# Kernel tuning notes

Measured on AMD Instinct MI355X. Metric: run time of the kernel, lower is better.

Reference implementation:

```python
import jax, jax.numpy as jnp
import numpy as np

N = 50000   # nodes
E = 800000  # edges
H = 128     # hidden_channels
L = 3       # num_layers - 2 GIN blocks
C = 1       # out_channels
G = 512     # graphs in batch
BN_EPS = 1e-5


def _bn(x, g, b, m, v):
    # BatchNorm1d in eval mode: running stats
    return g * (x - m) * jax.lax.rsqrt(v + BN_EPS) + b


def setup_inputs() -> dict:
    key = jax.random.key(0)
    ks = jax.random.split(key, 16)
    s = 0.05
    inp = {
        "x": jax.random.randint(ks[0], (N,), 0, 100),
        "edge_index": jax.random.randint(ks[1], (2, E), 0, N),
        "batch": jnp.sort(jax.random.randint(ks[2], (N,), 0, G)),
        "embed_table": jax.random.normal(ks[3], (100, H), jnp.float32) * s,
        # pre-conv BatchNorm1d (self.norms)
        "bn_g": jnp.ones((L, H), jnp.float32),
        "bn_b": jnp.zeros((L, H), jnp.float32),
        "bn_m": jax.random.normal(ks[4], (L, H), jnp.float32) * s,
        "bn_v": jax.random.uniform(ks[5], (L, H), jnp.float32, 0.5, 1.5),
        # self.lins
        "lin_w": jax.random.normal(ks[6], (L, H, H), jnp.float32) * s,
        "lin_b": jnp.zeros((L, H), jnp.float32),
        # GINConv eps (train_eps=True) and its MLP: Linear-BN-ReLU-Linear
        "eps": jnp.zeros((L,), jnp.float32),
        "mlp_w1": jax.random.normal(ks[7], (L, H, H), jnp.float32) * s,
        "mlp_b1": jnp.zeros((L, H), jnp.float32),
        "mbn_g": jnp.ones((L, H), jnp.float32),
        "mbn_b": jnp.zeros((L, H), jnp.float32),
        "mbn_m": jax.random.normal(ks[8], (L, H), jnp.float32) * s,
        "mbn_v": jax.random.uniform(ks[9], (L, H), jnp.float32, 0.5, 1.5),
        "mlp_w2": jax.random.normal(ks[10], (L, H, H), jnp.float32) * s,
        "mlp_b2": jnp.zeros((L, H), jnp.float32),
        # readout Linear
        "ro_w": jax.random.normal(ks[11], (H, C), jnp.float32) * s,
        "ro_b": jnp.zeros((C,), jnp.float32),
    }
    return inp


def reference(x, edge_index, batch, embed_table, bn_g, bn_b, bn_m, bn_v,
              lin_w, lin_b, eps, mlp_w1, mlp_b1, mbn_g, mbn_b, mbn_m, mbn_v,
              mlp_w2, mlp_b2, ro_w, ro_b):
    h = embed_table[x]                      # [N, H]
    src, dst = edge_index[0], edge_index[1]
    for i in range(L):
        h = _bn(h, bn_g[i], bn_b[i], bn_m[i], bn_v[i])
        h = jax.nn.relu(h @ lin_w[i] + lin_b[i])
        # dropout is identity in eval mode
        # GINConv: mlp((1+eps)*x + sum_{j in N(i)} x_j)
        agg = jax.ops.segment_sum(h[src], dst, num_segments=N)
        z = (1.0 + eps[i]) * h + agg
        z = jax.nn.relu(_bn(z @ mlp_w1[i] + mlp_b1[i], mbn_g[i], mbn_b[i], mbn_m[i], mbn_v[i]))
        h = z @ mlp_w2[i] + mlp_b2[i]
    out = h @ ro_w + ro_b                   # [N, C]
    return jax.ops.segment_sum(out, batch, num_segments=G)  # [G, C]
```

## Files before the change

kernel.cpp:

```cpp
#include <hip/hip_runtime.h>
#include <hip/hip_fp16.h>


#define HD 128
#define NLAYER 3
#define PITCH 136
#define EPB 2048

typedef _Float16 half8 __attribute__((ext_vector_type(8)));
typedef float    f32x4 __attribute__((ext_vector_type(4)));

__global__ void prep_weights(
    const float* __restrict__ bn_g, const float* __restrict__ bn_b,
    const float* __restrict__ bn_m, const float* __restrict__ bn_v,
    const float* __restrict__ lin_w, const float* __restrict__ lin_b,
    const float* __restrict__ mbn_g, const float* __restrict__ mbn_b,
    const float* __restrict__ mbn_m, const float* __restrict__ mbn_v,
    const float* __restrict__ mlp_w1, const float* __restrict__ mlp_b1,
    const float* __restrict__ mlp_w2,
    _Float16* __restrict__ wtl, float* __restrict__ fbl,
    _Float16* __restrict__ wt1, float* __restrict__ fb1,
    _Float16* __restrict__ wt2)
{
    const int l = blockIdx.x;
    const int t = threadIdx.x;
    __shared__ float sa[HD], sc[HD], sa2[HD];

    const int lb = l * HD;
    const int wb = l * HD * HD;
    float a  = bn_g[lb + t] * rsqrtf(bn_v[lb + t] + 1e-5f);
    float c  = bn_b[lb + t] - bn_m[lb + t] * a;
    float a2 = mbn_g[lb + t] * rsqrtf(mbn_v[lb + t] + 1e-5f);
    float c2 = mbn_b[lb + t] - mbn_m[lb + t] * a2;
    sa[t] = a; sc[t] = c; sa2[t] = a2;
    __syncthreads();

    float accb = lin_b[lb + t];
    for (int k = 0; k < HD; ++k) accb += sc[k] * lin_w[wb + k * HD + t];
    fbl[lb + t] = accb;
    fb1[lb + t] = a2 * mlp_b1[lb + t] + c2;

    for (int j = 0; j < HD; ++j) {
        wtl[wb + j * HD + t] = (_Float16)(sa[t] * lin_w[wb + t * HD + j]);
        wt1[wb + j * HD + t] = (_Float16)(sa2[j] * mlp_w1[wb + t * HD + j]);
        wt2[wb + j * HD + t] = (_Float16)(mlp_w2[wb + t * HD + j]);
    }
}

__global__ void count_deg(const int* __restrict__ dst, int* __restrict__ deg,
                          int e, int npr)
{
    int r = blockIdx.x & 7;
    int chunk = blockIdx.x >> 3;
    int lo = r * npr, hi = lo + npr;
    int base = chunk * EPB;
    int end = base + EPB; if (end > e) end = e;
    for (int i = base + threadIdx.x; i < end; i += 256) {
        int d = dst[i];
        if (d >= lo && d < hi) atomicAdd(&deg[d], 1);
    }
}

__global__ void fill_csr(const int* __restrict__ src, const int* __restrict__ dst,
                         int* __restrict__ cursor,
                         unsigned short* __restrict__ esrc, int e, int npr)
{
    int r = blockIdx.x & 7;
    int chunk = blockIdx.x >> 3;
    int lo = r * npr, hi = lo + npr;
    int base = chunk * EPB;
    int end = base + EPB; if (end > e) end = e;
    for (int i = base + threadIdx.x; i < end; i += 256) {
        int d = dst[i];
        int s = src[i];
        if (d >= lo && d < hi) {
            int p = atomicAdd(&cursor[d], 1);
            esrc[p] = (unsigned short)s;
        }
    }
}

__global__ void scan_blocks(const int* __restrict__ deg, int* __restrict__ excl,
                            int* __restrict__ partials, int n)
{
    __shared__ int wt[4];
    int t = threadIdx.x;
    int base = blockIdx.x * 1024 + t * 4;
    int v0 = (base + 0 < n) ? deg[base + 0] : 0;
    int v1 = (base + 1 < n) ? deg[base + 1] : 0;
    int v2 = (base + 2 < n) ? deg[base + 2] : 0;
    int v3 = (base + 3 < n) ? deg[base + 3] : 0;
    int s = v0 + v1 + v2 + v3;
    int lane = t & 63, w = t >> 6;
    int inc = s;
    #pragma unroll
    for (int d = 1; d < 64; d <<= 1) {
        int o = __shfl_up(inc, d);
        if (lane >= d) inc += o;
    }
    if (lane == 63) wt[w] = inc;
    __syncthreads();
    int off = 0;
    for (int i = 0; i < w; ++i) off += wt[i];
    int ex = off + inc - s;
    if (base + 0 < n) excl[base + 0] = ex; ex += v0;
    if (base + 1 < n) excl[base + 1] = ex; ex += v1;
    if (base + 2 < n) excl[base + 2] = ex; ex += v2;
    if (base + 3 < n) excl[base + 3] = ex;
    if (t == 255) partials[blockIdx.x] = off + inc;
}

__global__ void scan_small(int* __restrict__ partials, int nb)
{
    int t = threadIdx.x;
    int v = (t < nb) ? partials[t] : 0;
    int inc = v;
    #pragma unroll
    for (int d = 1; d < 64; d <<= 1) {
        int o = __shfl_up(inc, d);
        if (t >= d) inc += o;
    }
    if (t < nb) partials[t] = inc - v;
}

__global__ void scan_add(int* __restrict__ rowst, int* __restrict__ cursor,
                         const int* __restrict__ partials, int n, int e)
{
    int idx = blockIdx.x * blockDim.x + threadIdx.x;
    if (idx < n) {
        int v = rowst[idx] + partials[idx >> 10];
        rowst[idx] = v;
        cursor[idx] = v;
    }
    if (idx == 0) rowst[n] = e;
}

template<bool GATHER>
__global__ __launch_bounds__(256, 3)
void lin_mfma(const float* __restrict__ Xf, const _Float16* __restrict__ Xh,
              const int* __restrict__ xidx,
              const _Float16* __restrict__ Wt, const float* __restrict__ B,
              _Float16* __restrict__ Y, int n)
{
    __shared__ __align__(16) _Float16 sA[64 * PITCH];
    const int t = threadIdx.x;
    const int lane = t & 63;
    const int w = t >> 6;
    const int rw_ = w >> 1, cw = w & 1;
    const int m = lane & 15, g = lane >> 4;
    const int tile = blockIdx.x * 64;

    {
        int row = t >> 2, q = t & 3;
        int gr = tile + row;
        _Float16* dst = &sA[row * PITCH + q * 32];
        if (GATHER) {
            if (gr < n) {
                int id = xidx[gr];
                const float4* src = reinterpret_cast<const float4*>(Xf + (size_t)id * HD) + q * 8;
                #pragma unroll
                for (int c = 0; c < 4; ++c) {
                    float4 va = src[2 * c], vb = src[2 * c + 1];
                    half8 h = {(_Float16)va.x, (_Float16)va.y, (_Float16)va.z, (_Float16)va.w,
                               (_Float16)vb.x, (_Float16)vb.y, (_Float16)vb.z, (_Float16)vb.w};
                    *reinterpret_cast<half8*>(dst + c * 8) = h;
                }
            } else {
                half8 zz = {0, 0, 0, 0, 0, 0, 0, 0};
                #pragma unroll
                for (int c = 0; c < 4; ++c) *reinterpret_cast<half8*>(dst + c * 8) = zz;
            }
        } else {
            half8 zz = {0, 0, 0, 0, 0, 0, 0, 0};
            const half8* src = reinterpret_cast<const half8*>(Xh + (size_t)gr * HD + q * 32);
            #pragma unroll
            for (int c = 0; c < 4; ++c)
                *reinterpret_cast<half8*>(dst + c * 8) = (gr < n) ? src[c] : zz;
        }
    }
    __syncthreads();

    half8 bf[4][4];
    #pragma unroll
    for (int ct4 = 0; ct4 < 4; ++ct4) {
        int ct = 4 * cw + ct4;
        #pragma unroll
        for (int kk = 0; kk < 4; ++kk)
            bf[ct4][kk] = *reinterpret_cast<const half8*>(
                Wt + (size_t)(16 * ct + m) * HD + kk * 32 + g * 8);
    }

    f32x4 acc[2][4];
    #pragma unroll
    for (int i = 0; i < 2; ++i)
        #pragma unroll
        for (int j = 0; j < 4; ++j) acc[i][j] = (f32x4){0.f, 0.f, 0.f, 0.f};

    #pragma unroll
    for (int rg2 = 0; rg2 < 2; ++rg2) {
        int rg = 2 * rw_ + rg2;
        #pragma unroll
        for (int kk = 0; kk < 4; ++kk) {
            half8 a = *reinterpret_cast<const half8*>(
                &sA[(16 * rg + m) * PITCH + kk * 32 + g * 8]);
            #pragma unroll
            for (int ct4 = 0; ct4 < 4; ++ct4)
                acc[rg2][ct4] = __builtin_amdgcn_mfma_f32_16x16x32_f16(
                    a, bf[ct4][kk], acc[rg2][ct4], 0, 0, 0);
        }
    }

    #pragma unroll
    for (int rg2 = 0; rg2 < 2; ++rg2) {
        int rg = 2 * rw_ + rg2;
        #pragma unroll
        for (int ct4 = 0; ct4 < 4; ++ct4) {
            int col = 16 * (4 * cw + ct4) + m;
            float bb = B[col];
            #pragma unroll
            for (int reg = 0; reg < 4; ++reg) {
                int r = tile + 16 * rg + 4 * g + reg;
                if (r < n) {
                    float v = fmaxf(acc[rg2][ct4][reg] + bb, 0.f);
                    Y[(size_t)r * HD + col] = (_Float16)v;
                }
            }
        }
    }
}

__global__ void aggregate_f16(const _Float16* __restrict__ h2,
                              const int* __restrict__ rowst,
                              const unsigned short* __restrict__ esrc,
                              const float* __restrict__ epsp,
                              int layer, _Float16* __restrict__ z, int n)
{
    int gw = (blockIdx.x * blockDim.x + threadIdx.x) >> 6;
    int lane = threadIdx.x & 63;
    if (gw >= n) return;
    float se = 1.0f + epsp[layer];
    int rs = __builtin_amdgcn_readfirstlane(rowst[gw]);
    int re = __builtin_amdgcn_readfirstlane(rowst[gw + 1]);
    const half2* hv = reinterpret_cast<const half2*>(h2);
    float2 s = __half22float2(hv[(size_t)gw * 64 + lane]);
    float ax0 = se * s.x, ay0 = se * s.y;
    float ax1 = 0.f, ay1 = 0.f, ax2 = 0.f, ay2 = 0.f, ax3 = 0.f, ay3 = 0.f;
    for (int base = rs; base < re; base += 64) {
        int cnt = re - base; if (cnt > 64) cnt = 64;
        int eid = (base + lane < re) ? (int)esrc[base + lane] : 0;
        int j = 0;
        for (; j + 4 <= cnt; j += 4) {
            int s0 = __shfl(eid, j + 0);
            int s1 = __shfl(eid, j + 1);
            int s2 = __shfl(eid, j + 2);
            int s3 = __shfl(eid, j + 3);
            float2 v0 = __half22float2(hv[(size_t)s0 * 64 + lane]);
            float2 v1 = __half22float2(hv[(size_t)s1 * 64 + lane]);
            float2 v2 = __half22float2(hv[(size_t)s2 * 64 + lane]);
            float2 v3 = __half22float2(hv[(size_t)s3 * 64 + lane]);
            ax0 += v0.x; ay0 += v0.y;
            ax1 += v1.x; ay1 += v1.y;
            ax2 += v2.x; ay2 += v2.y;
            ax3 += v3.x; ay3 += v3.y;
        }
        for (; j < cnt; ++j) {
            int s0 = __shfl(eid, j);
            float2 v0 = __half22float2(hv[(size_t)s0 * 64 + lane]);
            ax0 += v0.x; ay0 += v0.y;
        }
    }
    float ox = (ax0 + ax1) + (ax2 + ax3);
    float oy = (ay0 + ay1) + (ay2 + ay3);
    reinterpret_cast<half2*>(z)[(size_t)gw * 64 + lane] = __floats2half2_rn(ox, oy);
}

template<bool FUSE_RO>
__global__ __launch_bounds__(256, 3)
void mlp_mfma(const _Float16* __restrict__ Z,
              const _Float16* __restrict__ Wt1, const float* __restrict__ B1,
              const _Float16* __restrict__ Wt2, const float* __restrict__ B2,
              _Float16* __restrict__ H,
              const float* __restrict__ rw, const float* __restrict__ rb,
              const int* __restrict__ batch, float* __restrict__ gout, int n)
{
    __shared__ __align__(16) _Float16 sA[64 * PITCH];
    __shared__ float sD[64][2];
    const int t = threadIdx.x;
    const int lane = t & 63;
    const int w = t >> 6;
    const int rw_ = w >> 1, cw = w & 1;
    const int m = lane & 15, g = lane >> 4;
    const int tile = blockIdx.x * 64;

    {
        int row = t >> 2, q = t & 3;
        int gr = tile + row;
        _Float16* dst = &sA[row * PITCH + q * 32];
        half8 zz = {0, 0, 0, 0, 0, 0, 0, 0};
        const half8* src = reinterpret_cast<const half8*>(Z + (size_t)gr * HD + q * 32);
        #pragma unroll
        for (int c = 0; c < 4; ++c)
            *reinterpret_cast<half8*>(dst + c * 8) = (gr < n) ? src[c] : zz;
    }
    __syncthreads();

    half8 bf[4][4];
    #pragma unroll
    for (int ct4 = 0; ct4 < 4; ++ct4) {
        int ct = 4 * cw + ct4;
        #pragma unroll
        for (int kk = 0; kk < 4; ++kk)
            bf[ct4][kk] = *reinterpret_cast<const half8*>(
                Wt1 + (size_t)(16 * ct + m) * HD + kk * 32 + g * 8);
    }
    f32x4 acc[2][4];
    #pragma unroll
    for (int i = 0; i < 2; ++i)
        #pragma unroll
        for (int j = 0; j < 4; ++j) acc[i][j] = (f32x4){0.f, 0.f, 0.f, 0.f};
    #pragma unroll
    for (int rg2 = 0; rg2 < 2; ++rg2) {
        int rg = 2 * rw_ + rg2;
        #pragma unroll
        for (int kk = 0; kk < 4; ++kk) {
            half8 a = *reinterpret_cast<const half8*>(
                &sA[(16 * rg + m) * PITCH + kk * 32 + g * 8]);
            #pragma unroll
            for (int ct4 = 0; ct4 < 4; ++ct4)
                acc[rg2][ct4] = __builtin_amdgcn_mfma_f32_16x16x32_f16(
                    a, bf[ct4][kk], acc[rg2][ct4], 0, 0, 0);
        }
    }
    __syncthreads();

    #pragma unroll
    for (int rg2 = 0; rg2 < 2; ++rg2) {
        int rg = 2 * rw_ + rg2;
        #pragma unroll
        for (int ct4 = 0; ct4 < 4; ++ct4) {
            int col = 16 * (4 * cw + ct4) + m;
            float bb = B1[col];
            #pragma unroll
            for (int reg = 0; reg < 4; ++reg) {
                int lr = 16 * rg + 4 * g + reg;
                sA[lr * PITCH + col] = (_Float16)fmaxf(acc[rg2][ct4][reg] + bb, 0.f);
            }
        }
    }
    __syncthreads();

    #pragma unroll
    for (int ct4 = 0; ct4 < 4; ++ct4) {
        int ct = 4 * cw + ct4;
        #pragma unroll
        for (int kk = 0; kk < 4; ++kk)
            bf[ct4][kk] = *reinterpret_cast<const half8*>(
                Wt2 + (size_t)(16 * ct + m) * HD + kk * 32 + g * 8);
    }
    f32x4 acc2[2][4];
    #pragma unroll
    for (int i = 0; i < 2; ++i)
        #pragma unroll
        for (int j = 0; j < 4; ++j) acc2[i][j] = (f32x4){0.f, 0.f, 0.f, 0.f};
    #pragma unroll
    for (int rg2 = 0; rg2 < 2; ++rg2) {
        int rg = 2 * rw_ + rg2;
        #pragma unroll
        for (int kk = 0; kk < 4; ++kk) {
            half8 a = *reinterpret_cast<const half8*>(
                &sA[(16 * rg + m) * PITCH + kk * 32 + g * 8]);
            #pragma unroll
            for (int ct4 = 0; ct4 < 4; ++ct4)
                acc2[rg2][ct4] = __builtin_amdgcn_mfma_f32_16x16x32_f16(
                    a, bf[ct4][kk], acc2[rg2][ct4], 0, 0, 0);
        }
    }

    if (!FUSE_RO) {
        #pragma unroll
        for (int rg2 = 0; rg2 < 2; ++rg2) {
            int rg = 2 * rw_ + rg2;
            #pragma unroll
            for (int ct4 = 0; ct4 < 4; ++ct4) {
                int col = 16 * (4 * cw + ct4) + m;
                float bb = B2[col];
                #pragma unroll
                for (int reg = 0; reg < 4; ++reg) {
                    int r = tile + 16 * rg + 4 * g + reg;
                    if (r < n)
                        H[(size_t)r * HD + col] = (_Float16)(acc2[rg2][ct4][reg] + bb);
                }
            }
        }
    } else {
        #pragma unroll
        for (int rg2 = 0; rg2 < 2; ++rg2) {
            int rg = 2 * rw_ + rg2;
            float pr[4] = {0.f, 0.f, 0.f, 0.f};
            #pragma unroll
            for (int ct4 = 0; ct4 < 4; ++ct4) {
                int col = 16 * (4 * cw + ct4) + m;
                float bb = B2[col], rr = rw[col];
                #pragma unroll
                for (int reg = 0; reg < 4; ++reg)
                    pr[reg] = fmaf(acc2[rg2][ct4][reg] + bb, rr, pr[reg]);
            }
            #pragma unroll
            for (int reg = 0; reg < 4; ++reg) {
                #pragma unroll
                for (int d = 1; d < 16; d <<= 1) pr[reg] += __shfl_xor(pr[reg], d);
            }
            if (m == 0) {
                #pragma unroll
                for (int reg = 0; reg < 4; ++reg)
                    sD[16 * rg + 4 * g + reg][cw] = pr[reg];
            }
        }
        __syncthreads();
        if (t < 64) {
            int row = tile + t;
            float v = sD[t][0] + sD[t][1] + rb[0];
            int b = (row < n) ? batch[row] : -1;
            if (row >= n) v = 0.f;
            #pragma unroll
            for (int d = 1; d < 64; d <<= 1) {
                int   ob = __shfl_up(b, d);
                float ov = __shfl_up(v, d);
                if (t >= d && ob == b) v += ov;
            }
            int nb2 = __shfl_down(b, 1);
            bool lastl = (t == 63) || (nb2 != b);
            if (lastl && b >= 0) atomicAdd(&gout[b], v);
        }
    }
}

extern "C" void kernel_launch(void* const* d_in, const int* in_sizes, int n_in,
                              void* d_out, int out_size, void* d_ws, size_t ws_size,
                              hipStream_t stream)
{
    const int N = in_sizes[0];
    const int E = in_sizes[1] / 2;
    const int G = out_size;

    const int*   x      = (const int*)d_in[0];
    const int*   ei     = (const int*)d_in[1];
    const int*   batch  = (const int*)d_in[2];
    const float* table  = (const float*)d_in[3];
    const float* bn_g   = (const float*)d_in[4];
    const float* bn_b   = (const float*)d_in[5];
    const float* bn_m   = (const float*)d_in[6];
    const float* bn_v   = (const float*)d_in[7];
    const float* lin_w  = (const float*)d_in[8];
    const float* lin_b  = (const float*)d_in[9];
    const float* epsv   = (const float*)d_in[10];
    const float* mlp_w1 = (const float*)d_in[11];
    const float* mlp_b1 = (const float*)d_in[12];
    const float* mbn_g  = (const float*)d_in[13];
    const float* mbn_b  = (const float*)d_in[14];
    const float* mbn_m  = (const float*)d_in[15];
    const float* mbn_v  = (const float*)d_in[16];
    const float* mlp_w2 = (const float*)d_in[17];
    const float* mlp_b2 = (const float*)d_in[18];
    const float* ro_w   = (const float*)d_in[19];
    const float* ro_b   = (const float*)d_in[20];

    const int* esrc_in = ei;
    const int* edst_in = ei + E;

    char* wsp = (char*)d_ws;
    size_t off = 0;
    auto alloc = [&](size_t bytes) {
        void* p = wsp + off;
        off += (bytes + 255) & ~(size_t)255;
        return p;
    };
    _Float16* bufA  = (_Float16*)alloc((size_t)N * HD * 2);
    _Float16* bufB  = (_Float16*)alloc((size_t)N * HD * 2);
    _Float16* wtl   = (_Float16*)alloc((size_t)NLAYER * HD * HD * 2);
    _Float16* wt1   = (_Float16*)alloc((size_t)NLAYER * HD * HD * 2);
    _Float16* wt2   = (_Float16*)alloc((size_t)NLAYER * HD * HD * 2);
    float*    fbl   = (float*)alloc((size_t)NLAYER * HD * 4);
    float*    fb1   = (float*)alloc((size_t)NLAYER * HD * 4);
    int*      deg   = (int*)alloc((size_t)N * 4);
    int*      rowst = (int*)alloc((size_t)(N + 1) * 4);
    int*      cursor= (int*)alloc((size_t)N * 4);
    unsigned short* esrc = (unsigned short*)alloc((size_t)E * 2);
    int*      part  = (int*)alloc(256 * 4);
    (void)ws_size;

    hipMemsetAsync(deg, 0, (size_t)N * 4, stream);
    hipMemsetAsync(d_out, 0, (size_t)G * 4, stream);

    prep_weights<<<NLAYER, HD, 0, stream>>>(
        bn_g, bn_b, bn_m, bn_v, lin_w, lin_b,
        mbn_g, mbn_b, mbn_m, mbn_v, mlp_w1, mlp_b1, mlp_w2,
        wtl, fbl, wt1, fb1, wt2);

    const int npr = (N + 7) / 8;
    const int chunks = (E + EPB - 1) / EPB;
    count_deg<<<chunks * 8, 256, 0, stream>>>(edst_in, deg, E, npr);
    int nb = (N + 1023) / 1024;
    scan_blocks<<<nb, 256, 0, stream>>>(deg, rowst, part, N);
    scan_small<<<1, 64, 0, stream>>>(part, nb);
    scan_add<<<(N + 255) / 256, 256, 0, stream>>>(rowst, cursor, part, N, E);
    fill_csr<<<chunks * 8, 256, 0, stream>>>(esrc_in, edst_in, cursor, esrc, E, npr);

    const int gemm_grid = (N + 63) / 64;
    const int wave_grid = (N + 3) / 4;

    for (int l = 0; l < NLAYER; ++l) {
        const _Float16* wl = wtl + (size_t)l * HD * HD;
        const float*    bl = fbl + (size_t)l * HD;
        const _Float16* w1 = wt1 + (size_t)l * HD * HD;
        const float*    b1 = fb1 + (size_t)l * HD;
        const _Float16* w2 = wt2 + (size_t)l * HD * HD;
        const float*    b2 = mlp_b2 + (size_t)l * HD;

        if (l == 0)
            lin_mfma<true><<<gemm_grid, 256, 0, stream>>>(
                table, nullptr, x, wl, bl, bufB, N);
        else
            lin_mfma<false><<<gemm_grid, 256, 0, stream>>>(
                nullptr, bufA, nullptr, wl, bl, bufB, N);

        aggregate_f16<<<wave_grid, 256, 0, stream>>>(
            bufB, rowst, esrc, epsv, l, bufA, N);

        if (l < NLAYER - 1)
            mlp_mfma<false><<<gemm_grid, 256, 0, stream>>>(
                bufA, w1, b1, w2, b2, bufA,
                nullptr, nullptr, nullptr, nullptr, N);
        else
            mlp_mfma<true><<<gemm_grid, 256, 0, stream>>>(
                bufA, w1, b1, w2, b2, nullptr,
                ro_w, ro_b, batch, (float*)d_out, N);
    }
}
```

Baseline: 410.9 us.

## Fuse neighbor aggregation into MLP kernel, gathering directly into shared memory

Removes the separate aggregate kernel. The MLP GEMM kernel now performs the CSR neighbor gather itself: each wave aggregates 16 nodes and writes the sums straight into the shared A tile, which avoids writing the intermediate z to global memory and reading it back. The inner gather loop is also unrolled from 4 to 8 independent loads. In exchange, each GEMM block runs the aggregation serially over 16 nodes per wave with only 3 blocks per CU, so memory-latency hiding for the gather may drop compared with the wave-per-node kernel.

```diff
diff --git a/kernel.cpp b/kernel.cpp
--- a/kernel.cpp
+++ b/kernel.cpp
@@ -8,6 +8,7 @@
 #define EPB 2048
 
 typedef _Float16 half8 __attribute__((ext_vector_type(8)));
+typedef _Float16 half2f __attribute__((ext_vector_type(2)));
 typedef float    f32x4 __attribute__((ext_vector_type(4)));
 
 __global__ void prep_weights(
@@ -229,59 +230,16 @@
     }
 }
 
-__global__ void aggregate_f16(const _Float16* __restrict__ h2,
-                              const int* __restrict__ rowst,
-                              const unsigned short* __restrict__ esrc,
-                              const float* __restrict__ epsp,
-                              int layer, _Float16* __restrict__ z, int n)
-{
-    int gw = (blockIdx.x * blockDim.x + threadIdx.x) >> 6;
-    int lane = threadIdx.x & 63;
-    if (gw >= n) return;
-    float se = 1.0f + epsp[layer];
-    int rs = __builtin_amdgcn_readfirstlane(rowst[gw]);
-    int re = __builtin_amdgcn_readfirstlane(rowst[gw + 1]);
-    const half2* hv = reinterpret_cast<const half2*>(h2);
-    float2 s = __half22float2(hv[(size_t)gw * 64 + lane]);
-    float ax0 = se * s.x, ay0 = se * s.y;
-    float ax1 = 0.f, ay1 = 0.f, ax2 = 0.f, ay2 = 0.f, ax3 = 0.f, ay3 = 0.f;
-    for (int base = rs; base < re; base += 64) {
-        int cnt = re - base; if (cnt > 64) cnt = 64;
-        int eid = (base + lane < re) ? (int)esrc[base + lane] : 0;
-        int j = 0;
-        for (; j + 4 <= cnt; j += 4) {
-            int s0 = __shfl(eid, j + 0);
-            int s1 = __shfl(eid, j + 1);
-            int s2 = __shfl(eid, j + 2);
-            int s3 = __shfl(eid, j + 3);
-            float2 v0 = __half22float2(hv[(size_t)s0 * 64 + lane]);
-            float2 v1 = __half22float2(hv[(size_t)s1 * 64 + lane]);
-            float2 v2 = __half22float2(hv[(size_t)s2 * 64 + lane]);
-            float2 v3 = __half22float2(hv[(size_t)s3 * 64 + lane]);
-            ax0 += v0.x; ay0 += v0.y;
-            ax1 += v1.x; ay1 += v1.y;
-            ax2 += v2.x; ay2 += v2.y;
-            ax3 += v3.x; ay3 += v3.y;
-        }
-        for (; j < cnt; ++j) {
-            int s0 = __shfl(eid, j);
-            float2 v0 = __half22float2(hv[(size_t)s0 * 64 + lane]);
-            ax0 += v0.x; ay0 += v0.y;
-        }
-    }
-    float ox = (ax0 + ax1) + (ax2 + ax3);
-    float oy = (ay0 + ay1) + (ay2 + ay3);
-    reinterpret_cast<half2*>(z)[(size_t)gw * 64 + lane] = __floats2half2_rn(ox, oy);
-}
-
 template<bool FUSE_RO>
 __global__ __launch_bounds__(256, 3)
-void mlp_mfma(const _Float16* __restrict__ Z,
-              const _Float16* __restrict__ Wt1, const float* __restrict__ B1,
-              const _Float16* __restrict__ Wt2, const float* __restrict__ B2,
-              _Float16* __restrict__ H,
-              const float* __restrict__ rw, const float* __restrict__ rb,
-              const int* __restrict__ batch, float* __restrict__ gout, int n)
+void aggmlp(const _Float16* __restrict__ h2,
+            const int* __restrict__ rowst, const unsigned short* __restrict__ esrc,
+            const float* __restrict__ epsp, int layer,
+            const _Float16* __restrict__ Wt1, const float* __restrict__ B1,
+            const _Float16* __restrict__ Wt2, const float* __restrict__ B2,
+            _Float16* __restrict__ H,
+            const float* __restrict__ rw, const float* __restrict__ rb,
+            const int* __restrict__ batch, float* __restrict__ gout, int n)
 {
     __shared__ __align__(16) _Float16 sA[64 * PITCH];
     __shared__ float sD[64][2];
@@ -293,14 +251,56 @@
     const int tile = blockIdx.x * 64;
 
     {
-        int row = t >> 2, q = t & 3;
-        int gr = tile + row;
-        _Float16* dst = &sA[row * PITCH + q * 32];
-        half8 zz = {0, 0, 0, 0, 0, 0, 0, 0};
-        const half8* src = reinterpret_cast<const half8*>(Z + (size_t)gr * HD + q * 32);
-        #pragma unroll
-        for (int c = 0; c < 4; ++c)
-            *reinterpret_cast<half8*>(dst + c * 8) = (gr < n) ? src[c] : zz;
+        const half2* hv = reinterpret_cast<const half2*>(h2);
+        const float se = 1.0f + epsp[layer];
+        for (int rr = 0; rr < 16; ++rr) {
+            int node = tile + 16 * w + rr;
+            float ox = 0.f, oy = 0.f;
+            if (node < n) {
+                int rs = __builtin_amdgcn_readfirstlane(rowst[node]);
+                int re = __builtin_amdgcn_readfirstlane(rowst[node + 1]);
+                float2 own = __half22float2(hv[(size_t)node * 64 + lane]);
+                float ax0 = se * own.x, ay0 = se * own.y;
+                float ax1 = 0.f, ay1 = 0.f, ax2 = 0.f, ay2 = 0.f, ax3 = 0.f, ay3 = 0.f;
+                float ax4 = 0.f, ay4 = 0.f, ax5 = 0.f, ay5 = 0.f, ax6 = 0.f, ay6 = 0.f, ax7 = 0.f, ay7 = 0.f;
+                for (int base = rs; base < re; base += 64) {
+                    int cnt = re - base; if (cnt > 64) cnt = 64;
+                    int eid = (base + lane < re) ? (int)esrc[base + lane] : 0;
+                    int j = 0;
+                    for (; j + 8 <= cnt; j += 8) {
+                        int s0 = __shfl(eid, j + 0);
+                        int s1 = __shfl(eid, j + 1);
+                        int s2 = __shfl(eid, j + 2);
+                        int s3 = __shfl(eid, j + 3);
+                        int s4 = __shfl(eid, j + 4);
+                        int s5 = __shfl(eid, j + 5);
+                        int s6 = __shfl(eid, j + 6);
+                        int s7 = __shfl(eid, j + 7);
+                        float2 v0 = __half22float2(hv[(size_t)s0 * 64 + lane]);
+                        float2 v1 = __half22float2(hv[(size_t)s1 * 64 + lane]);
+                        float2 v2 = __half22float2(hv[(size_t)s2 * 64 + lane]);
+                        float2 v3 = __half22float2(hv[(size_t)s3 * 64 + lane]);
+                        float2 v4 = __half22float2(hv[(size_t)s4 * 64 + lane]);
+                        float2 v5 = __half22float2(hv[(size_t)s5 * 64 + lane]);
+                        float2 v6 = __half22float2(hv[(size_t)s6 * 64 + lane]);
+                        float2 v7 = __half22float2(hv[(size_t)s7 * 64 + lane]);
+                        ax0 += v0.x; ay0 += v0.y;  ax1 += v1.x; ay1 += v1.y;
+                        ax2 += v2.x; ay2 += v2.y;  ax3 += v3.x; ay3 += v3.y;
+                        ax4 += v4.x; ay4 += v4.y;  ax5 += v5.x; ay5 += v5.y;
+                        ax6 += v6.x; ay6 += v6.y;  ax7 += v7.x; ay7 += v7.y;
+                    }
+                    for (; j < cnt; ++j) {
+                        int s0 = __shfl(eid, j);
+                        float2 v0 = __half22float2(hv[(size_t)s0 * 64 + lane]);
+                        ax0 += v0.x; ay0 += v0.y;
+                    }
+                }
+                ox = ((ax0 + ax1) + (ax2 + ax3)) + ((ax4 + ax5) + (ax6 + ax7));
+                oy = ((ay0 + ay1) + (ay2 + ay3)) + ((ay4 + ay5) + (ay6 + ay7));
+            }
+            *reinterpret_cast<half2f*>(&sA[(16 * w + rr) * PITCH + 2 * lane]) =
+                (half2f){(_Float16)ox, (_Float16)oy};
+        }
     }
     __syncthreads();
 
@@ -507,7 +507,6 @@
     fill_csr<<<chunks * 8, 256, 0, stream>>>(esrc_in, edst_in, cursor, esrc, E, npr);
 
     const int gemm_grid = (N + 63) / 64;
-    const int wave_grid = (N + 3) / 4;
 
     for (int l = 0; l < NLAYER; ++l) {
         const _Float16* wl = wtl + (size_t)l * HD * HD;
@@ -524,16 +523,13 @@
             lin_mfma<false><<<gemm_grid, 256, 0, stream>>>(
                 nullptr, bufA, nullptr, wl, bl, bufB, N);
 
-        aggregate_f16<<<wave_grid, 256, 0, stream>>>(
-            bufB, rowst, esrc, epsv, l, bufA, N);
-
         if (l < NLAYER - 1)
-            mlp_mfma<false><<<gemm_grid, 256, 0, stream>>>(
-                bufA, w1, b1, w2, b2, bufA,
+            aggmlp<false><<<gemm_grid, 256, 0, stream>>>(
+                bufB, rowst, esrc, epsv, l, w1, b1, w2, b2, bufA,
                 nullptr, nullptr, nullptr, nullptr, N);
         else
-            mlp_mfma<true><<<gemm_grid, 256, 0, stream>>>(
-                bufA, w1, b1, w2, b2, nullptr,
+            aggmlp<true><<<gemm_grid, 256, 0, stream>>>(
+                bufB, rowst, esrc, epsv, l, w1, b1, w2, b2, nullptr,
                 ro_w, ro_b, batch, (float*)d_out, N);
     }
 }
```

Result: slower. 463.6 us (+12.8%).

## Fuse next layer's linear into MLP kernel and unroll aggregation by eight

Applied to the files above, without the earlier changes.

The MLP kernel now also applies the next layer's BN-folded linear plus ReLU. It stages the second GEMM's output in shared memory and runs a third MFMA GEMM, so the separate lin_mfma launches for layers 1 and 2 go away. This removes one full N×H fp16 write and read round trip per fused layer. The aggregation inner loop is unrolled from 4 to 8 independent gathers to put more loads in flight, at the cost of more registers. The scan partials buffer is also enlarged.

```diff
diff --git a/kernel.cpp b/kernel.cpp
--- a/kernel.cpp
+++ b/kernel.cpp
@@ -135,10 +135,8 @@
     if (idx == 0) rowst[n] = e;
 }
 
-template<bool GATHER>
 __global__ __launch_bounds__(256, 3)
-void lin_mfma(const float* __restrict__ Xf, const _Float16* __restrict__ Xh,
-              const int* __restrict__ xidx,
+void lin_mfma(const float* __restrict__ Xf, const int* __restrict__ xidx,
               const _Float16* __restrict__ Wt, const float* __restrict__ B,
               _Float16* __restrict__ Y, int n)
 {
@@ -154,28 +152,20 @@
         int row = t >> 2, q = t & 3;
         int gr = tile + row;
         _Float16* dst = &sA[row * PITCH + q * 32];
-        if (GATHER) {
-            if (gr < n) {
-                int id = xidx[gr];
-                const float4* src = reinterpret_cast<const float4*>(Xf + (size_t)id * HD) + q * 8;
-                #pragma unroll
-                for (int c = 0; c < 4; ++c) {
-                    float4 va = src[2 * c], vb = src[2 * c + 1];
-                    half8 h = {(_Float16)va.x, (_Float16)va.y, (_Float16)va.z, (_Float16)va.w,
-                               (_Float16)vb.x, (_Float16)vb.y, (_Float16)vb.z, (_Float16)vb.w};
-                    *reinterpret_cast<half8*>(dst + c * 8) = h;
-                }
-            } else {
-                half8 zz = {0, 0, 0, 0, 0, 0, 0, 0};
-                #pragma unroll
-                for (int c = 0; c < 4; ++c) *reinterpret_cast<half8*>(dst + c * 8) = zz;
+        if (gr < n) {
+            int id = xidx[gr];
+            const float4* src = reinterpret_cast<const float4*>(Xf + (size_t)id * HD) + q * 8;
+            #pragma unroll
+            for (int c = 0; c < 4; ++c) {
+                float4 va = src[2 * c], vb = src[2 * c + 1];
+                half8 h = {(_Float16)va.x, (_Float16)va.y, (_Float16)va.z, (_Float16)va.w,
+                           (_Float16)vb.x, (_Float16)vb.y, (_Float16)vb.z, (_Float16)vb.w};
+                *reinterpret_cast<half8*>(dst + c * 8) = h;
             }
         } else {
             half8 zz = {0, 0, 0, 0, 0, 0, 0, 0};
-            const half8* src = reinterpret_cast<const half8*>(Xh + (size_t)gr * HD + q * 32);
-            #pragma unroll
-            for (int c = 0; c < 4; ++c)
-                *reinterpret_cast<half8*>(dst + c * 8) = (gr < n) ? src[c] : zz;
+            #pragma unroll
+            for (int c = 0; c < 4; ++c) *reinterpret_cast<half8*>(dst + c * 8) = zz;
         }
     }
     __syncthreads();
@@ -245,23 +235,32 @@
     float2 s = __half22float2(hv[(size_t)gw * 64 + lane]);
     float ax0 = se * s.x, ay0 = se * s.y;
     float ax1 = 0.f, ay1 = 0.f, ax2 = 0.f, ay2 = 0.f, ax3 = 0.f, ay3 = 0.f;
+    float ax4 = 0.f, ay4 = 0.f, ax5 = 0.f, ay5 = 0.f, ax6 = 0.f, ay6 = 0.f, ax7 = 0.f, ay7 = 0.f;
     for (int base = rs; base < re; base += 64) {
         int cnt = re - base; if (cnt > 64) cnt = 64;
         int eid = (base + lane < re) ? (int)esrc[base + lane] : 0;
         int j = 0;
-        for (; j + 4 <= cnt; j += 4) {
+        for (; j + 8 <= cnt; j += 8) {
             int s0 = __shfl(eid, j + 0);
             int s1 = __shfl(eid, j + 1);
             int s2 = __shfl(eid, j + 2);
             int s3 = __shfl(eid, j + 3);
+            int s4 = __shfl(eid, j + 4);
+            int s5 = __shfl(eid, j + 5);
+            int s6 = __shfl(eid, j + 6);
+            int s7 = __shfl(eid, j + 7);
             float2 v0 = __half22float2(hv[(size_t)s0 * 64 + lane]);
             float2 v1 = __half22float2(hv[(size_t)s1 * 64 + lane]);
             float2 v2 = __half22float2(hv[(size_t)s2 * 64 + lane]);
             float2 v3 = __half22float2(hv[(size_t)s3 * 64 + lane]);
-            ax0 += v0.x; ay0 += v0.y;
-            ax1 += v1.x; ay1 += v1.y;
-            ax2 += v2.x; ay2 += v2.y;
-            ax3 += v3.x; ay3 += v3.y;
+            float2 v4 = __half22float2(hv[(size_t)s4 * 64 + lane]);
+            float2 v5 = __half22float2(hv[(size_t)s5 * 64 + lane]);
+            float2 v6 = __half22float2(hv[(size_t)s6 * 64 + lane]);
+            float2 v7 = __half22float2(hv[(size_t)s7 * 64 + lane]);
+            ax0 += v0.x; ay0 += v0.y;  ax1 += v1.x; ay1 += v1.y;
+            ax2 += v2.x; ay2 += v2.y;  ax3 += v3.x; ay3 += v3.y;
+            ax4 += v4.x; ay4 += v4.y;  ax5 += v5.x; ay5 += v5.y;
+            ax6 += v6.x; ay6 += v6.y;  ax7 += v7.x; ay7 += v7.y;
         }
         for (; j < cnt; ++j) {
             int s0 = __shfl(eid, j);
@@ -269,19 +268,20 @@
             ax0 += v0.x; ay0 += v0.y;
         }
     }
-    float ox = (ax0 + ax1) + (ax2 + ax3);
-    float oy = (ay0 + ay1) + (ay2 + ay3);
+    float ox = ((ax0 + ax1) + (ax2 + ax3)) + ((ax4 + ax5) + (ax6 + ax7));
+    float oy = ((ay0 + ay1) + (ay2 + ay3)) + ((ay4 + ay5) + (ay6 + ay7));
     reinterpret_cast<half2*>(z)[(size_t)gw * 64 + lane] = __floats2half2_rn(ox, oy);
 }
 
-template<bool FUSE_RO>
+template<bool LAST>
 __global__ __launch_bounds__(256, 3)
-void mlp_mfma(const _Float16* __restrict__ Z,
-              const _Float16* __restrict__ Wt1, const float* __restrict__ B1,
-              const _Float16* __restrict__ Wt2, const float* __restrict__ B2,
-              _Float16* __restrict__ H,
-              const float* __restrict__ rw, const float* __restrict__ rb,
-              const int* __restrict__ batch, float* __restrict__ gout, int n)
+void mlp3(const _Float16* __restrict__ Z,
+          const _Float16* __restrict__ Wt1, const float* __restrict__ B1,
+          const _Float16* __restrict__ Wt2, const float* __restrict__ B2,
+          const _Float16* __restrict__ Wt3, const float* __restrict__ B3,
+          _Float16* __restrict__ Y,
+          const float* __restrict__ rw, const float* __restrict__ rb,
+          const int* __restrict__ batch, float* __restrict__ gout, int n)
 {
     __shared__ __align__(16) _Float16 sA[64 * PITCH];
     __shared__ float sD[64][2];
@@ -305,6 +305,8 @@
     __syncthreads();
 
     half8 bf[4][4];
+    f32x4 acc[2][4];
+
     #pragma unroll
     for (int ct4 = 0; ct4 < 4; ++ct4) {
         int ct = 4 * cw + ct4;
@@ -313,7 +315,6 @@
             bf[ct4][kk] = *reinterpret_cast<const half8*>(
                 Wt1 + (size_t)(16 * ct + m) * HD + kk * 32 + g * 8);
     }
-    f32x4 acc[2][4];
     #pragma unroll
     for (int i = 0; i < 2; ++i)
         #pragma unroll
@@ -332,7 +333,6 @@
         }
     }
     __syncthreads();
-
     #pragma unroll
     for (int rg2 = 0; rg2 < 2; ++rg2) {
         int rg = 2 * rw_ + rg2;
@@ -376,23 +376,7 @@
         }
     }
 
-    if (!FUSE_RO) {
-        #pragma unroll
-        for (int rg2 = 0; rg2 < 2; ++rg2) {
-            int rg = 2 * rw_ + rg2;
-            #pragma unroll
-            for (int ct4 = 0; ct4 < 4; ++ct4) {
-                int col = 16 * (4 * cw + ct4) + m;
-                float bb = B2[col];
-                #pragma unroll
-                for (int reg = 0; reg < 4; ++reg) {
-                    int r = tile + 16 * rg + 4 * g + reg;
-                    if (r < n)
-                        H[(size_t)r * HD + col] = (_Float16)(acc2[rg2][ct4][reg] + bb);
-                }
-            }
-        }
-    } else {
+    if (LAST) {
         #pragma unroll
         for (int rg2 = 0; rg2 < 2; ++rg2) {
             int rg = 2 * rw_ + rg2;
@@ -431,6 +415,66 @@
             int nb2 = __shfl_down(b, 1);
             bool lastl = (t == 63) || (nb2 != b);
             if (lastl && b >= 0) atomicAdd(&gout[b], v);
+        }
+    } else {
+        __syncthreads();
+        #pragma unroll
+        for (int rg2 = 0; rg2 < 2; ++rg2) {
+            int rg = 2 * rw_ + rg2;
+            #pragma unroll
+            for (int ct4 = 0; ct4 < 4; ++ct4) {
+                int col = 16 * (4 * cw + ct4) + m;
+                float bb = B2[col];
+                #pragma unroll
+                for (int reg = 0; reg < 4; ++reg) {
+                    int lr = 16 * rg + 4 * g + reg;
+                    sA[lr * PITCH + col] = (_Float16)(acc2[rg2][ct4][reg] + bb);
+                }
+            }
+        }
+        __syncthreads();
+
+        #pragma unroll
+        for (int ct4 = 0; ct4 < 4; ++ct4) {
+            int ct = 4 * cw + ct4;
+            #pragma unroll
+            for (int kk = 0; kk < 4; ++kk)
+                bf[ct4][kk] = *reinterpret_cast<const half8*>(
+                    Wt3 + (size_t)(16 * ct + m) * HD + kk * 32 + g * 8);
+        }
+        #pragma unroll
+        for (int i = 0; i < 2; ++i)
+            #pragma unroll
+            for (int j = 0; j < 4; ++j) acc[i][j] = (f32x4){0.f, 0.f, 0.f, 0.f};
+        #pragma unroll
+        for (int rg2 = 0; rg2 < 2; ++rg2) {
+            int rg = 2 * rw_ + rg2;
+            #pragma unroll
+            for (int kk = 0; kk < 4; ++kk) {
+                half8 a = *reinterpret_cast<const half8*>(
+                    &sA[(16 * rg + m) * PITCH + kk * 32 + g * 8]);
+                #pragma unroll
+                for (int ct4 = 0; ct4 < 4; ++ct4)
+                    acc[rg2][ct4] = __builtin_amdgcn_mfma_f32_16x16x32_f16(
+                        a, bf[ct4][kk], acc[rg2][ct4], 0, 0, 0);
+            }
+        }
+        #pragma unroll
+        for (int rg2 = 0; rg2 < 2; ++rg2) {
+            int rg = 2 * rw_ + rg2;
+            #pragma unroll
+            for (int ct4 = 0; ct4 < 4; ++ct4) {
+                int col = 16 * (4 * cw + ct4) + m;
+                float bb = B3[col];
+                #pragma unroll
+                for (int reg = 0; reg < 4; ++reg) {
+                    int r = tile + 16 * rg + 4 * g + reg;
+                    if (r < n) {
+                        float v = fmaxf(acc[rg2][ct4][reg] + bb, 0.f);
+                        Y[(size_t)r * HD + col] = (_Float16)v;
+                    }
+                }
+            }
         }
     }
 }
@@ -486,7 +530,7 @@
     int*      rowst = (int*)alloc((size_t)(N + 1) * 4);
     int*      cursor= (int*)alloc((size_t)N * 4);
     unsigned short* esrc = (unsigned short*)alloc((size_t)E * 2);
-    int*      part  = (int*)alloc(256 * 4);
+    int*      part  = (int*)alloc(1024 * 4);
     (void)ws_size;
 
     hipMemsetAsync(deg, 0, (size_t)N * 4, stream);
@@ -509,31 +553,27 @@
     const int gemm_grid = (N + 63) / 64;
     const int wave_grid = (N + 3) / 4;
 
+    lin_mfma<<<gemm_grid, 256, 0, stream>>>(table, x, wtl, fbl, bufB, N);
+
     for (int l = 0; l < NLAYER; ++l) {
-        const _Float16* wl = wtl + (size_t)l * HD * HD;
-        const float*    bl = fbl + (size_t)l * HD;
         const _Float16* w1 = wt1 + (size_t)l * HD * HD;
         const float*    b1 = fb1 + (size_t)l * HD;
         const _Float16* w2 = wt2 + (size_t)l * HD * HD;
         const float*    b2 = mlp_b2 + (size_t)l * HD;
 
-        if (l == 0)
-            lin_mfma<true><<<gemm_grid, 256, 0, stream>>>(
-                table, nullptr, x, wl, bl, bufB, N);
-        else
-            lin_mfma<false><<<gemm_grid, 256, 0, stream>>>(
-                nullptr, bufA, nullptr, wl, bl, bufB, N);
-
         aggregate_f16<<<wave_grid, 256, 0, stream>>>(
             bufB, rowst, esrc, epsv, l, bufA, N);
 
-        if (l < NLAYER - 1)
-            mlp_mfma<false><<<gemm_grid, 256, 0, stream>>>(
-                bufA, w1, b1, w2, b2, bufA,
+        if (l < NLAYER - 1) {
+            const _Float16* w3 = wtl + (size_t)(l + 1) * HD * HD;
+            const float*    b3 = fbl + (size_t)(l + 1) * HD;
+            mlp3<false><<<gemm_grid, 256, 0, stream>>>(
+                bufA, w1, b1, w2, b2, w3, b3, bufB,
                 nullptr, nullptr, nullptr, nullptr, N);
-        else
-            mlp_mfma<true><<<gemm_grid, 256, 0, stream>>>(
-                bufA, w1, b1, w2, b2, nullptr,
+        } else {
+            mlp3<true><<<gemm_grid, 256, 0, stream>>>(
+                bufA, w1, b1, w2, b2, nullptr, nullptr, nullptr,
                 ro_w, ro_b, batch, (float*)d_out, N);
-    }
-}
+        }
+    }
+}
```

Result: faster. 399.5 us (-2.8%).
